# Performance work log

Hardware: AMD Instinct MI355X
Metric: run time of the kernel (lower is better)

## Reference

```python
import jax, jax.numpy as jnp
import numpy as np

D_MODEL = 1024
N_EXPERTS = 8
TOP_K = 2
B, S = 2, 2048


def setup_inputs() -> dict:
    key = jax.random.key(0)
    ks = jax.random.split(key, 12)
    d, e, h = D_MODEL, N_EXPERTS, 4 * D_MODEL
    sd = 1.0 / np.sqrt(d)
    sh = 1.0 / np.sqrt(h)
    return {
        "x": jax.random.normal(ks[0], (B, S, d), dtype=jnp.float32),
        "noise": jax.random.uniform(ks[1], (B, S, e), dtype=jnp.float32),
        # router linear [d, E]
        "Wr": jax.random.uniform(ks[2], (d, e), minval=-sd, maxval=sd),
        "br": jax.random.uniform(ks[3], (e,), minval=-sd, maxval=sd),
        # noise linear [d, E]
        "Wn": jax.random.uniform(ks[4], (d, e), minval=-sd, maxval=sd),
        "bn": jax.random.uniform(ks[5], (e,), minval=-sd, maxval=sd),
        # stacked expert FFN weights
        "W1": jax.random.uniform(ks[6], (e, d, h), minval=-sd, maxval=sd),
        "b1": jax.random.uniform(ks[7], (e, h), minval=-sd, maxval=sd),
        "W2": jax.random.uniform(ks[8], (e, h, d), minval=-sh, maxval=sh),
        "b2": jax.random.uniform(ks[9], (e, d), minval=-sh, maxval=sh),
    }


def _moe_forward(x, noise, Wr, br, Wn, bn, W1, b1, W2, b2):
    e = Wr.shape[-1]
    # noisy top-k router
    logits = x @ Wr + br + jax.nn.softplus(x @ Wn + bn) * noise  # [B,S,E]
    top_v, top_i = jax.lax.top_k(logits, TOP_K)                  # [B,S,K]
    # softmax over sparse top-k (non-topk entries are -inf -> weight 0)
    gates_k = jax.nn.softmax(top_v, axis=-1)                     # [B,S,K]
    gating = jnp.sum(jax.nn.one_hot(top_i, e, dtype=x.dtype) * gates_k[..., None], axis=-2)  # [B,S,E]
    # experts (dropout in eval mode = identity). Non-selected experts have
    # gate 0, so the dense weighted sum equals the masked gather/scatter.
    hdn = jax.nn.relu(jnp.einsum('bsd,edh->bseh', x, W1) + b1)   # [B,S,E,4d]
    y = jnp.einsum('bseh,ehd->bsed', hdn, W2) + b2               # [B,S,E,d]
    return jnp.einsum('bse,bsed->bsd', gating, y)


def reference(x, noise, Wr, br, Wn, bn, W1, b1, W2, b2):
    return _moe_forward(x, noise, Wr, br, Wn, bn, W1, b1, W2, b2)
```

## Files before the change

kernel.cpp:

```cpp
#include <hip/hip_runtime.h>
#include <hip/hip_bf16.h>
#include <cstdint>
#include <cstddef>

#define D_MODEL 1024
#define N_EXP   8
#define HID     4096
#define T_TOK   4096
#define NPAIR   (T_TOK * 2)
#define WSLOTS  72

#define WS_COUNTS   0
#define WS_CURSOR   32
#define WS_OFFSETS  64
#define WS_TOKE     128
#define WS_TOKG     32896
#define WS_LTOK     65664
#define WS_LGATE    98432
#define WS_XB       131328
#define WS_WB       (WS_XB + 8388608)
#define WS_H        (WS_WB + 67108864)

typedef __attribute__((ext_vector_type(8))) short bf16x8;
typedef __attribute__((ext_vector_type(4))) float f32x4;
typedef __attribute__((ext_vector_type(8))) unsigned short u16x8;
typedef unsigned short u16;

__device__ __forceinline__ u16 f2bf(float f) {
    unsigned u = __float_as_uint(f);
    u += 0x7FFFu + ((u >> 16) & 1u);
    return (u16)(u >> 16);
}

__device__ __forceinline__ void glds16(const void* g, void* l) {
    __builtin_amdgcn_global_load_lds(
        (const __attribute__((address_space(1))) void*)g,
        (__attribute__((address_space(3))) void*)l, 16, 0, 0);
}

__device__ __forceinline__ void chunk_map(int c, int& row, int& kc) {
    const int line = c >> 3, c8 = c & 7, u = c8 ^ (line & 7);
    row = line * 2 + (u >> 2);
    kc  = (u & 3) * 8;
}

__device__ __forceinline__ bool work_map(const int* counts, int w,
                                         int& e, int& m_t) {
    int tot = 0; e = -1; m_t = 0;
    #pragma unroll
    for (int i = 0; i < N_EXP; ++i) {
        const int tl = (counts[i] + 127) >> 7;
        if (e < 0 && w < tot + tl) { e = i; m_t = w - tot; }
        tot += tl;
    }
    return e >= 0;
}

__global__ __launch_bounds__(256) void k_router(
    const float* __restrict__ x, const float* __restrict__ noise,
    const float* __restrict__ Wr, const float* __restrict__ br,
    const float* __restrict__ Wn, const float* __restrict__ bn,
    int* __restrict__ counts, int* __restrict__ tok_e, float* __restrict__ tok_g,
    u16* __restrict__ xb)
{
    const int t   = blockIdx.x;
    const int tid = threadIdx.x;
    const int e   = tid & 7;
    const int g   = tid >> 3;
    const float* xr = x + (size_t)t * D_MODEL;

    {
        const float4 v4 = *(const float4*)(xr + tid * 4);
        ushort4 o;
        o.x = f2bf(v4.x); o.y = f2bf(v4.y); o.z = f2bf(v4.z); o.w = f2bf(v4.w);
        *(ushort4*)(xb + (size_t)t * D_MODEL + tid * 4) = o;
    }

    float ar = 0.f, an = 0.f;
    const int ibase = g * 32;
    #pragma unroll 8
    for (int j = 0; j < 32; ++j) {
        const int i = ibase + j;
        const float xv = xr[i];
        ar = fmaf(xv, Wr[i * 8 + e], ar);
        an = fmaf(xv, Wn[i * 8 + e], an);
    }

    __shared__ float sR[256], sN[256];
    sR[tid] = ar; sN[tid] = an;
    __syncthreads();
    for (int off = 128; off >= 8; off >>= 1) {
        if (tid < off) { sR[tid] += sR[tid + off]; sN[tid] += sN[tid + off]; }
        __syncthreads();
    }

    __shared__ float lg[8];
    if (tid < 8) {
        const float z  = sN[tid] + bn[tid];
        const float sp = fmaxf(z, 0.f) + log1pf(expf(-fabsf(z)));
        lg[tid] = sR[tid] + br[tid] + sp * noise[t * 8 + tid];
    }
    __syncthreads();

    if (tid == 0) {
        float v0 = -INFINITY, v1 = -INFINITY;
        int   i0 = 0,         i1 = 0;
        #pragma unroll
        for (int ee = 0; ee < 8; ++ee) {
            const float v = lg[ee];
            if (v > v0)      { v1 = v0; i1 = i0; v0 = v; i0 = ee; }
            else if (v > v1) { v1 = v;  i1 = ee; }
        }
        const float ew  = expf(v1 - v0);
        const float inv = 1.f / (1.f + ew);
        tok_e[t * 2 + 0] = i0;
        tok_e[t * 2 + 1] = i1;
        tok_g[t * 2 + 0] = inv;
        tok_g[t * 2 + 1] = ew * inv;
        atomicAdd(&counts[i0], 1);
        atomicAdd(&counts[i1], 1);
    }
}

__global__ void k_prefix(const int* __restrict__ counts, int* __restrict__ offsets)
{
    if (threadIdx.x == 0 && blockIdx.x == 0) {
        int acc = 0;
        #pragma unroll
        for (int e = 0; e < N_EXP; ++e) { offsets[e] = acc; acc += counts[e]; }
    }
}

__global__ __launch_bounds__(256) void k_scatter(
    const int* __restrict__ tok_e, const float* __restrict__ tok_g,
    const int* __restrict__ offsets, int* __restrict__ cursor,
    int* __restrict__ list_tok, float* __restrict__ list_gate)
{
    const int gid = blockIdx.x * 256 + threadIdx.x;
    if (gid >= NPAIR) return;
    const int e = tok_e[gid];
    const int p = atomicAdd(&cursor[e], 1);
    const int slot = offsets[e] + p;
    list_tok[slot]  = gid >> 1;
    list_gate[slot] = tok_g[gid];
}

__global__ __launch_bounds__(256) void k_cvtT(
    const float* __restrict__ in, u16* __restrict__ outp, int R, int C)
{
    const size_t esz = (size_t)R * C;
    const float* ine = in + (size_t)blockIdx.z * esz;
    u16* oute = outp + (size_t)blockIdx.z * esz;
    const int c0 = blockIdx.x * 32, r0 = blockIdx.y * 64;

    __shared__ u16 s[64 * 33];
    const int tid = threadIdx.x;
    const int lr = tid >> 3, lc = (tid & 7) * 4;
    #pragma unroll
    for (int p = 0; p < 2; ++p) {
        const int row = lr + p * 32;
        const float4 v = *(const float4*)(ine + (size_t)(r0 + row) * C + c0 + lc);
        s[row * 33 + lc + 0] = f2bf(v.x);
        s[row * 33 + lc + 1] = f2bf(v.y);
        s[row * 33 + lc + 2] = f2bf(v.z);
        s[row * 33 + lc + 3] = f2bf(v.w);
    }
    __syncthreads();
    const int oc = tid >> 3, rr = (tid & 7) * 8;
    u16x8 o;
    #pragma unroll
    for (int i = 0; i < 8; ++i) o[i] = s[(rr + i) * 33 + oc];
    *(u16x8*)(oute + (size_t)(c0 + oc) * R + r0 + rr) = o;
}

__global__ __launch_bounds__(256, 4) void k_ffn1(
    const u16* __restrict__ xb,
    const u16* __restrict__ W1t,
    const float* __restrict__ b1,
    const int* __restrict__ counts, const int* __restrict__ offsets,
    const int* __restrict__ list_tok,
    u16* __restrict__ H)
{
    const int bid = blockIdx.x;
    const int n_t = (bid & 7) | (((bid >> 3) & 3) << 3);
    const int wsl = bid >> 5;

    int e, m_t;
    if (!work_map(counts, wsl, e, m_t)) return;
    const int cnt  = counts[e];
    const int base = offsets[e];
    const int m0   = m_t * 128;
    const int n0   = n_t * 128;
    const u16* __restrict__ Be = W1t + (size_t)e * (HID * D_MODEL);

    __shared__ __align__(16) u16 SA[2 * 4096];
    __shared__ __align__(16) u16 SB[2 * 4096];
    __shared__ int stok[128];

    const int tid = threadIdx.x;
    if (tid < 128) stok[tid] = list_tok[base + min(m0 + tid, cnt - 1)];
    __syncthreads();

    int ar0, ak0, ar1, ak1;
    chunk_map(tid, ar0, ak0);
    chunk_map(tid + 256, ar1, ak1);
    const u16* Asrc0 = xb + (size_t)stok[ar0] * D_MODEL + ak0;
    const u16* Asrc1 = xb + (size_t)stok[ar1] * D_MODEL + ak1;
    const u16* Bsrc0 = Be + (size_t)(n0 + ar0) * D_MODEL + ak0;
    const u16* Bsrc1 = Be + (size_t)(n0 + ar1) * D_MODEL + ak1;

    const int lane = tid & 63, lr = lane & 15, hk = lane >> 4;
    const int w = tid >> 6, wm = w >> 1, wn = w & 1;
    const int colb  = ((((lr & 1) << 2) + hk) ^ (lr >> 1)) << 4;
    const int baseA = ((wm * 32 + (lr >> 1)) << 7) + colb;
    const int baseB = ((wn * 32 + (lr >> 1)) << 7) + colb;

    float bias[4];
    #pragma unroll
    for (int j = 0; j < 4; ++j) bias[j] = b1[(size_t)e * HID + n0 + wn * 64 + j * 16 + lr];

    f32x4 acc[4][4] = {};

    auto STAGE = [&](int s, int t) {
        const int kt = t * 32;
        char* Ab = (char*)SA + s * 8192;
        char* Bb = (char*)SB + s * 8192;
        glds16(Asrc0 + kt, Ab + tid * 16);
        glds16(Asrc1 + kt, Ab + (tid + 256) * 16);
        glds16(Bsrc0 + kt, Bb + tid * 16);
        glds16(Bsrc1 + kt, Bb + (tid + 256) * 16);
    };
    auto COMPUTE = [&](int s) {
        const char* Ab = (const char*)SA + s * 8192;
        const char* Bb = (const char*)SB + s * 8192;
        bf16x8 a[4], b[4];
        #pragma unroll
        for (int i = 0; i < 4; ++i) a[i] = *(const bf16x8*)(Ab + baseA + i * 1024);
        #pragma unroll
        for (int j = 0; j < 4; ++j) b[j] = *(const bf16x8*)(Bb + baseB + j * 1024);
        #pragma unroll
        for (int i = 0; i < 4; ++i)
            #pragma unroll
            for (int j = 0; j < 4; ++j)
                acc[i][j] = __builtin_amdgcn_mfma_f32_16x16x32_bf16(a[i], b[j], acc[i][j], 0, 0, 0);
    };

    const int NT = D_MODEL / 32;
    STAGE(0, 0);
    STAGE(1, 1);
    for (int t = 0; t < NT; ++t) {
        if (t < NT - 1) { asm volatile("s_waitcnt vmcnt(4)" ::: "memory"); }
        else            { asm volatile("s_waitcnt vmcnt(0)" ::: "memory"); }
        __builtin_amdgcn_s_barrier();
        __builtin_amdgcn_sched_barrier(0);
        COMPUTE(t & 1);
        __builtin_amdgcn_sched_barrier(0);
        __builtin_amdgcn_s_barrier();
        if (t + 2 < NT) STAGE(t & 1, t + 2);
    }

    #pragma unroll
    for (int i = 0; i < 4; ++i) {
        #pragma unroll
        for (int g = 0; g < 4; ++g) {
            const int m = m0 + wm * 64 + i * 16 + hk * 4 + g;
            if (m < cnt) {
                u16* dst = H + (size_t)(base + m) * HID + n0 + wn * 64 + lr;
                #pragma unroll
                for (int j = 0; j < 4; ++j)
                    dst[j * 16] = f2bf(fmaxf(acc[i][j][g] + bias[j], 0.f));
            }
        }
    }
}

__global__ __launch_bounds__(256, 4) void k_ffn2(
    const u16* __restrict__ Hb,
    const u16* __restrict__ W2t,
    const float* __restrict__ b2,
    const int* __restrict__ counts, const int* __restrict__ offsets,
    const int* __restrict__ list_tok, const float* __restrict__ list_gate,
    float* __restrict__ out)
{
    const int bid = blockIdx.x;
    const int n_t = bid & 7;
    const int wsl = bid >> 3;

    int e, m_t;
    if (!work_map(counts, wsl, e, m_t)) return;
    const int cnt  = counts[e];
    const int base = offsets[e];
    const int m0   = m_t * 128;
    const int n0   = n_t * 128;
    const u16* __restrict__ Be = W2t + (size_t)e * (D_MODEL * HID);

    __shared__ __align__(16) u16 SA[2 * 4096];
    __shared__ __align__(16) u16 SB[2 * 4096];
    __shared__ int   s_tok[128];
    __shared__ float s_gate[128];

    const int tid = threadIdx.x;
    if (tid < 128) {
        const int sl = base + min(m0 + tid, cnt - 1);
        s_tok[tid]  = list_tok[sl];
        s_gate[tid] = list_gate[sl];
    }
    __syncthreads();

    int ar0, ak0, ar1, ak1;
    chunk_map(tid, ar0, ak0);
    chunk_map(tid + 256, ar1, ak1);
    const u16* Asrc0 = Hb + (size_t)(base + min(m0 + ar0, cnt - 1)) * HID + ak0;
    const u16* Asrc1 = Hb + (size_t)(base + min(m0 + ar1, cnt - 1)) * HID + ak1;
    const u16* Bsrc0 = Be + (size_t)(n0 + ar0) * HID + ak0;
    const u16* Bsrc1 = Be + (size_t)(n0 + ar1) * HID + ak1;

    const int lane = tid & 63, lr = lane & 15, hk = lane >> 4;
    const int w = tid >> 6, wm = w >> 1, wn = w & 1;
    const int colb  = ((((lr & 1) << 2) + hk) ^ (lr >> 1)) << 4;
    const int baseA = ((wm * 32 + (lr >> 1)) << 7) + colb;
    const int baseB = ((wn * 32 + (lr >> 1)) << 7) + colb;

    float bias[4];
    #pragma unroll
    for (int j = 0; j < 4; ++j) bias[j] = b2[(size_t)e * D_MODEL + n0 + wn * 64 + j * 16 + lr];

    f32x4 acc[4][4] = {};

    auto STAGE = [&](int s, int t) {
        const int kt = t * 32;
        char* Ab = (char*)SA + s * 8192;
        char* Bb = (char*)SB + s * 8192;
        glds16(Asrc0 + kt, Ab + tid * 16);
        glds16(Asrc1 + kt, Ab + (tid + 256) * 16);
        glds16(Bsrc0 + kt, Bb + tid * 16);
        glds16(Bsrc1 + kt, Bb + (tid + 256) * 16);
    };
    auto COMPUTE = [&](int s) {
        const char* Ab = (const char*)SA + s * 8192;
        const char* Bb = (const char*)SB + s * 8192;
        bf16x8 a[4], b[4];
        #pragma unroll
        for (int i = 0; i < 4; ++i) a[i] = *(const bf16x8*)(Ab + baseA + i * 1024);
        #pragma unroll
        for (int j = 0; j < 4; ++j) b[j] = *(const bf16x8*)(Bb + baseB + j * 1024);
        #pragma unroll
        for (int i = 0; i < 4; ++i)
            #pragma unroll
            for (int j = 0; j < 4; ++j)
                acc[i][j] = __builtin_amdgcn_mfma_f32_16x16x32_bf16(a[i], b[j], acc[i][j], 0, 0, 0);
    };

    const int NT = HID / 32;
    STAGE(0, 0);
    STAGE(1, 1);
    for (int t = 0; t < NT; ++t) {
        if (t < NT - 1) { asm volatile("s_waitcnt vmcnt(4)" ::: "memory"); }
        else            { asm volatile("s_waitcnt vmcnt(0)" ::: "memory"); }
        __builtin_amdgcn_s_barrier();
        __builtin_amdgcn_sched_barrier(0);
        COMPUTE(t & 1);
        __builtin_amdgcn_sched_barrier(0);
        __builtin_amdgcn_s_barrier();
        if (t + 2 < NT) STAGE(t & 1, t + 2);
    }

    #pragma unroll
    for (int i = 0; i < 4; ++i) {
        #pragma unroll
        for (int g = 0; g < 4; ++g) {
            const int m = m0 + wm * 64 + i * 16 + hk * 4 + g;
            if (m < cnt) {
                const int   mm = m - m0;
                const int   tk = s_tok[mm];
                const float gt = s_gate[mm];
                float* dst = out + (size_t)tk * D_MODEL + n0 + wn * 64 + lr;
                #pragma unroll
                for (int j = 0; j < 4; ++j)
                    unsafeAtomicAdd(dst + j * 16, gt * (acc[i][j][g] + bias[j]));
            }
        }
    }
}

extern "C" void kernel_launch(void* const* d_in, const int* in_sizes, int n_in,
                              void* d_out, int out_size, void* d_ws, size_t ws_size,
                              hipStream_t stream)
{
    const float* x     = (const float*)d_in[0];
    const float* noise = (const float*)d_in[1];
    const float* Wr    = (const float*)d_in[2];
    const float* br    = (const float*)d_in[3];
    const float* Wn    = (const float*)d_in[4];
    const float* bn    = (const float*)d_in[5];
    const float* W1    = (const float*)d_in[6];
    const float* b1    = (const float*)d_in[7];
    const float* W2    = (const float*)d_in[8];
    const float* b2    = (const float*)d_in[9];
    float* out = (float*)d_out;

    char* ws = (char*)d_ws;
    int*   counts    = (int*)(ws + WS_COUNTS);
    int*   cursor    = (int*)(ws + WS_CURSOR);
    int*   offsets   = (int*)(ws + WS_OFFSETS);
    int*   tok_e     = (int*)(ws + WS_TOKE);
    float* tok_g     = (float*)(ws + WS_TOKG);
    int*   list_tok  = (int*)(ws + WS_LTOK);
    float* list_gate = (float*)(ws + WS_LGATE);
    u16*   xb        = (u16*)(ws + WS_XB);
    u16*   Wb        = (u16*)(ws + WS_WB);
    u16*   Hb        = (u16*)(ws + WS_H);

    hipMemsetAsync(ws, 0, 128, stream);
    hipMemsetAsync(d_out, 0, (size_t)out_size * sizeof(float), stream);

    k_cvtT<<<dim3(HID / 32, D_MODEL / 64, N_EXP), 256, 0, stream>>>(W1, Wb, D_MODEL, HID);
    k_router<<<T_TOK, 256, 0, stream>>>(x, noise, Wr, br, Wn, bn, counts, tok_e, tok_g, xb);
    k_prefix<<<1, 64, 0, stream>>>(counts, offsets);
    k_scatter<<<NPAIR / 256, 256, 0, stream>>>(tok_e, tok_g, offsets, cursor,
                                               list_tok, list_gate);

    k_ffn1<<<32 * WSLOTS, 256, 0, stream>>>(xb, Wb, b1, counts, offsets,
                                            list_tok, Hb);

    k_cvtT<<<dim3(D_MODEL / 32, HID / 64, N_EXP), 256, 0, stream>>>(W2, Wb, HID, D_MODEL);
    k_ffn2<<<8 * WSLOTS, 256, 0, stream>>>(Hb, Wb, b2, counts, offsets,
                                           list_tok, list_gate, out);
}
```

Before: 453.9 us.

## Enlarge FFN1 M-tile to 256 with 512 threads; deepen FFN2 K-step to 64

FFN1 now gives each block 256 token rows with 8 waves sharing one 128-column weight tile, so each W1 tile loaded into LDS is reused across twice as many tokens. FFN2 stages 64-wide K slices with a new XOR swizzle and makes two MFMA sub-steps per barrier, halving the number of barrier and wait rounds. The cost is more LDS per block, lower occupancy (launch bounds drop to 2 blocks per CU), and more padded rows wasted per expert when counts are not multiples of 256.

```diff
diff --git a/kernel.cpp b/kernel.cpp
--- a/kernel.cpp
+++ b/kernel.cpp
@@ -9,6 +9,7 @@
 #define T_TOK   4096
 #define NPAIR   (T_TOK * 2)
 #define WSLOTS  72
+#define WSL256  40
 
 #define WS_COUNTS   0
 #define WS_CURSOR   32
@@ -44,12 +45,24 @@
     kc  = (u & 3) * 8;
 }
 
+
 __device__ __forceinline__ bool work_map(const int* counts, int w,
                                          int& e, int& m_t) {
     int tot = 0; e = -1; m_t = 0;
     #pragma unroll
     for (int i = 0; i < N_EXP; ++i) {
         const int tl = (counts[i] + 127) >> 7;
+        if (e < 0 && w < tot + tl) { e = i; m_t = w - tot; }
+        tot += tl;
+    }
+    return e >= 0;
+}
+__device__ __forceinline__ bool work_map256(const int* counts, int w,
+                                            int& e, int& m_t) {
+    int tot = 0; e = -1; m_t = 0;
+    #pragma unroll
+    for (int i = 0; i < N_EXP; ++i) {
+        const int tl = (counts[i] + 255) >> 8;
         if (e < 0 && w < tot + tl) { e = i; m_t = w - tot; }
         tot += tl;
     }
@@ -173,7 +186,7 @@
     *(u16x8*)(oute + (size_t)(c0 + oc) * R + r0 + rr) = o;
 }
 
-__global__ __launch_bounds__(256, 4) void k_ffn1(
+__global__ __launch_bounds__(512, 2) void k_ffn1(
     const u16* __restrict__ xb,
     const u16* __restrict__ W1t,
     const float* __restrict__ b1,
@@ -186,28 +199,27 @@
     const int wsl = bid >> 5;
 
     int e, m_t;
-    if (!work_map(counts, wsl, e, m_t)) return;
+    if (!work_map256(counts, wsl, e, m_t)) return;
     const int cnt  = counts[e];
     const int base = offsets[e];
-    const int m0   = m_t * 128;
+    const int m0   = m_t * 256;
     const int n0   = n_t * 128;
     const u16* __restrict__ Be = W1t + (size_t)e * (HID * D_MODEL);
 
-    __shared__ __align__(16) u16 SA[2 * 4096];
+    __shared__ __align__(16) u16 SA[2 * 8192];
     __shared__ __align__(16) u16 SB[2 * 4096];
-    __shared__ int stok[128];
+    __shared__ int stok[256];
 
     const int tid = threadIdx.x;
-    if (tid < 128) stok[tid] = list_tok[base + min(m0 + tid, cnt - 1)];
+    if (tid < 256) stok[tid] = list_tok[base + min(m0 + tid, cnt - 1)];
     __syncthreads();
 
     int ar0, ak0, ar1, ak1;
     chunk_map(tid, ar0, ak0);
-    chunk_map(tid + 256, ar1, ak1);
+    chunk_map(tid + 512, ar1, ak1);
     const u16* Asrc0 = xb + (size_t)stok[ar0] * D_MODEL + ak0;
     const u16* Asrc1 = xb + (size_t)stok[ar1] * D_MODEL + ak1;
-    const u16* Bsrc0 = Be + (size_t)(n0 + ar0) * D_MODEL + ak0;
-    const u16* Bsrc1 = Be + (size_t)(n0 + ar1) * D_MODEL + ak1;
+    const u16* Bsrc  = Be + (size_t)(n0 + ar0) * D_MODEL + ak0;
 
     const int lane = tid & 63, lr = lane & 15, hk = lane >> 4;
     const int w = tid >> 6, wm = w >> 1, wn = w & 1;
@@ -223,16 +235,15 @@
 
     auto STAGE = [&](int s, int t) {
         const int kt = t * 32;
-        char* Ab = (char*)SA + s * 8192;
-        char* Bb = (char*)SB + s * 8192;
+        char* Ab = (char*)(SA + s * 8192);
+        char* Bb = (char*)(SB + s * 4096);
         glds16(Asrc0 + kt, Ab + tid * 16);
-        glds16(Asrc1 + kt, Ab + (tid + 256) * 16);
-        glds16(Bsrc0 + kt, Bb + tid * 16);
-        glds16(Bsrc1 + kt, Bb + (tid + 256) * 16);
+        glds16(Asrc1 + kt, Ab + (tid + 512) * 16);
+        glds16(Bsrc  + kt, Bb + tid * 16);
     };
     auto COMPUTE = [&](int s) {
-        const char* Ab = (const char*)SA + s * 8192;
-        const char* Bb = (const char*)SB + s * 8192;
+        const char* Ab = (const char*)(SA + s * 8192);
+        const char* Bb = (const char*)(SB + s * 4096);
         bf16x8 a[4], b[4];
         #pragma unroll
         for (int i = 0; i < 4; ++i) a[i] = *(const bf16x8*)(Ab + baseA + i * 1024);
@@ -249,7 +260,7 @@
     STAGE(0, 0);
     STAGE(1, 1);
     for (int t = 0; t < NT; ++t) {
-        if (t < NT - 1) { asm volatile("s_waitcnt vmcnt(4)" ::: "memory"); }
+        if (t < NT - 1) { asm volatile("s_waitcnt vmcnt(3)" ::: "memory"); }
         else            { asm volatile("s_waitcnt vmcnt(0)" ::: "memory"); }
         __builtin_amdgcn_s_barrier();
         __builtin_amdgcn_sched_barrier(0);
@@ -274,7 +285,7 @@
     }
 }
 
-__global__ __launch_bounds__(256, 4) void k_ffn2(
+__global__ __launch_bounds__(256, 2) void k_ffn2(
     const u16* __restrict__ Hb,
     const u16* __restrict__ W2t,
     const float* __restrict__ b2,
@@ -294,8 +305,8 @@
     const int n0   = n_t * 128;
     const u16* __restrict__ Be = W2t + (size_t)e * (D_MODEL * HID);
 
-    __shared__ __align__(16) u16 SA[2 * 4096];
-    __shared__ __align__(16) u16 SB[2 * 4096];
+    __shared__ __align__(16) u16 SA[2 * 8192];
+    __shared__ __align__(16) u16 SB[2 * 8192];
     __shared__ int   s_tok[128];
     __shared__ float s_gate[128];
 
@@ -307,19 +318,21 @@
     }
     __syncthreads();
 
-    int ar0, ak0, ar1, ak1;
-    chunk_map(tid, ar0, ak0);
-    chunk_map(tid + 256, ar1, ak1);
-    const u16* Asrc0 = Hb + (size_t)(base + min(m0 + ar0, cnt - 1)) * HID + ak0;
-    const u16* Asrc1 = Hb + (size_t)(base + min(m0 + ar1, cnt - 1)) * HID + ak1;
-    const u16* Bsrc0 = Be + (size_t)(n0 + ar0) * HID + ak0;
-    const u16* Bsrc1 = Be + (size_t)(n0 + ar1) * HID + ak1;
+    const u16* Asrc[4];
+    const u16* Bsrc[4];
+    #pragma unroll
+    for (int g = 0; g < 4; ++g) {
+        const int s = g * 256 + tid;
+        const int r = s >> 3;
+        const int u = (s & 7) ^ (r & 7);
+        Asrc[g] = Hb + (size_t)(base + min(m0 + r, cnt - 1)) * HID + u * 8;
+        Bsrc[g] = Be + (size_t)(n0 + r) * HID + u * 8;
+    }
 
     const int lane = tid & 63, lr = lane & 15, hk = lane >> 4;
     const int w = tid >> 6, wm = w >> 1, wn = w & 1;
-    const int colb  = ((((lr & 1) << 2) + hk) ^ (lr >> 1)) << 4;
-    const int baseA = ((wm * 32 + (lr >> 1)) << 7) + colb;
-    const int baseB = ((wn * 32 + (lr >> 1)) << 7) + colb;
+    const int baseA = (wm * 64 + lr) * 128 + ((hk ^ (lr & 7)) << 4);
+    const int baseB = (wn * 64 + lr) * 128 + ((hk ^ (lr & 7)) << 4);
 
     float bias[4];
     #pragma unroll
@@ -328,34 +341,38 @@
     f32x4 acc[4][4] = {};
 
     auto STAGE = [&](int s, int t) {
-        const int kt = t * 32;
-        char* Ab = (char*)SA + s * 8192;
-        char* Bb = (char*)SB + s * 8192;
-        glds16(Asrc0 + kt, Ab + tid * 16);
-        glds16(Asrc1 + kt, Ab + (tid + 256) * 16);
-        glds16(Bsrc0 + kt, Bb + tid * 16);
-        glds16(Bsrc1 + kt, Bb + (tid + 256) * 16);
+        const int kt = t * 64;
+        char* Ab = (char*)(SA + s * 8192);
+        char* Bb = (char*)(SB + s * 8192);
+        #pragma unroll
+        for (int g = 0; g < 4; ++g) glds16(Asrc[g] + kt, Ab + (g * 256 + tid) * 16);
+        #pragma unroll
+        for (int g = 0; g < 4; ++g) glds16(Bsrc[g] + kt, Bb + (g * 256 + tid) * 16);
     };
     auto COMPUTE = [&](int s) {
-        const char* Ab = (const char*)SA + s * 8192;
-        const char* Bb = (const char*)SB + s * 8192;
-        bf16x8 a[4], b[4];
-        #pragma unroll
-        for (int i = 0; i < 4; ++i) a[i] = *(const bf16x8*)(Ab + baseA + i * 1024);
-        #pragma unroll
-        for (int j = 0; j < 4; ++j) b[j] = *(const bf16x8*)(Bb + baseB + j * 1024);
-        #pragma unroll
-        for (int i = 0; i < 4; ++i)
+        const char* Ab = (const char*)(SA + s * 8192);
+        const char* Bb = (const char*)(SB + s * 8192);
+        #pragma unroll
+        for (int ks = 0; ks < 2; ++ks) {
+            const int kx = ks * 64;
+            bf16x8 a[4], b[4];
             #pragma unroll
-            for (int j = 0; j < 4; ++j)
-                acc[i][j] = __builtin_amdgcn_mfma_f32_16x16x32_bf16(a[i], b[j], acc[i][j], 0, 0, 0);
+            for (int i = 0; i < 4; ++i) a[i] = *(const bf16x8*)(Ab + ((baseA + i * 2048) ^ kx));
+            #pragma unroll
+            for (int j = 0; j < 4; ++j) b[j] = *(const bf16x8*)(Bb + ((baseB + j * 2048) ^ kx));
+            #pragma unroll
+            for (int i = 0; i < 4; ++i)
+                #pragma unroll
+                for (int j = 0; j < 4; ++j)
+                    acc[i][j] = __builtin_amdgcn_mfma_f32_16x16x32_bf16(a[i], b[j], acc[i][j], 0, 0, 0);
+        }
     };
 
-    const int NT = HID / 32;
+    const int NT = HID / 64;
     STAGE(0, 0);
     STAGE(1, 1);
     for (int t = 0; t < NT; ++t) {
-        if (t < NT - 1) { asm volatile("s_waitcnt vmcnt(4)" ::: "memory"); }
+        if (t < NT - 1) { asm volatile("s_waitcnt vmcnt(8)" ::: "memory"); }
         else            { asm volatile("s_waitcnt vmcnt(0)" ::: "memory"); }
         __builtin_amdgcn_s_barrier();
         __builtin_amdgcn_sched_barrier(0);
@@ -420,7 +437,7 @@
     k_scatter<<<NPAIR / 256, 256, 0, stream>>>(tok_e, tok_g, offsets, cursor,
                                                list_tok, list_gate);
 
-    k_ffn1<<<32 * WSLOTS, 256, 0, stream>>>(xb, Wb, b1, counts, offsets,
+    k_ffn1<<<32 * WSL256, 512, 0, stream>>>(xb, Wb, b1, counts, offsets,
                                             list_tok, Hb);
 
     k_cvtT<<<dim3(D_MODEL / 32, HID / 64, N_EXP), 256, 0, stream>>>(W2, Wb, HID, D_MODEL);
```

Result: slower. 502.8 us (+10.8%).

## Fuse fp32 weight conversion into expert GEMM B-tile loads

Applied to the files above, without the earlier changes.

Removes the two separate transpose-and-convert kernels that wrote bf16 copies of W1 and W2 to workspace. The FFN GEMMs now read fp32 weights directly through registers, pack them to bf16 with v_cvt_pk_bf16_f32 and write a padded LDS tile, pipelined one stage ahead. This avoids a full extra read and write pass over both weight tensors per call. In exchange, the GEMMs read weights at twice the byte width, every M-tile block repeats the conversion, and register and LDS pressure rise.

```diff
diff --git a/kernel.cpp b/kernel.cpp
--- a/kernel.cpp
+++ b/kernel.cpp
@@ -18,12 +18,10 @@
 #define WS_LTOK     65664
 #define WS_LGATE    98432
 #define WS_XB       131328
-#define WS_WB       (WS_XB + 8388608)
-#define WS_H        (WS_WB + 67108864)
+#define WS_H        (WS_XB + 8388608)
 
 typedef __attribute__((ext_vector_type(8))) short bf16x8;
 typedef __attribute__((ext_vector_type(4))) float f32x4;
-typedef __attribute__((ext_vector_type(8))) unsigned short u16x8;
 typedef unsigned short u16;
 
 __device__ __forceinline__ u16 f2bf(float f) {
@@ -145,37 +143,10 @@
     list_gate[slot] = tok_g[gid];
 }
 
-__global__ __launch_bounds__(256) void k_cvtT(
-    const float* __restrict__ in, u16* __restrict__ outp, int R, int C)
-{
-    const size_t esz = (size_t)R * C;
-    const float* ine = in + (size_t)blockIdx.z * esz;
-    u16* oute = outp + (size_t)blockIdx.z * esz;
-    const int c0 = blockIdx.x * 32, r0 = blockIdx.y * 64;
-
-    __shared__ u16 s[64 * 33];
-    const int tid = threadIdx.x;
-    const int lr = tid >> 3, lc = (tid & 7) * 4;
-    #pragma unroll
-    for (int p = 0; p < 2; ++p) {
-        const int row = lr + p * 32;
-        const float4 v = *(const float4*)(ine + (size_t)(r0 + row) * C + c0 + lc);
-        s[row * 33 + lc + 0] = f2bf(v.x);
-        s[row * 33 + lc + 1] = f2bf(v.y);
-        s[row * 33 + lc + 2] = f2bf(v.z);
-        s[row * 33 + lc + 3] = f2bf(v.w);
-    }
-    __syncthreads();
-    const int oc = tid >> 3, rr = (tid & 7) * 8;
-    u16x8 o;
-    #pragma unroll
-    for (int i = 0; i < 8; ++i) o[i] = s[(rr + i) * 33 + oc];
-    *(u16x8*)(oute + (size_t)(c0 + oc) * R + r0 + rr) = o;
-}
 
 __global__ __launch_bounds__(256, 4) void k_ffn1(
     const u16* __restrict__ xb,
-    const u16* __restrict__ W1t,
+    const float* __restrict__ W1,
     const float* __restrict__ b1,
     const int* __restrict__ counts, const int* __restrict__ offsets,
     const int* __restrict__ list_tok,
@@ -191,10 +162,10 @@
     const int base = offsets[e];
     const int m0   = m_t * 128;
     const int n0   = n_t * 128;
-    const u16* __restrict__ Be = W1t + (size_t)e * (HID * D_MODEL);
+    const float* __restrict__ Bw = W1 + (size_t)e * (D_MODEL * HID);
 
     __shared__ __align__(16) u16 SA[2 * 4096];
-    __shared__ __align__(16) u16 SB[2 * 4096];
+    __shared__ __align__(16) u16 SBl[2 * 5120];
     __shared__ int stok[128];
 
     const int tid = threadIdx.x;
@@ -206,38 +177,61 @@
     chunk_map(tid + 256, ar1, ak1);
     const u16* Asrc0 = xb + (size_t)stok[ar0] * D_MODEL + ak0;
     const u16* Asrc1 = xb + (size_t)stok[ar1] * D_MODEL + ak1;
-    const u16* Bsrc0 = Be + (size_t)(n0 + ar0) * D_MODEL + ak0;
-    const u16* Bsrc1 = Be + (size_t)(n0 + ar1) * D_MODEL + ak1;
+
+    const int kq = tid & 7;
+    const int nq = tid >> 3;
+    const float* Bbase = Bw + (size_t)(4 * kq) * HID + n0 + nq * 4;
 
     const int lane = tid & 63, lr = lane & 15, hk = lane >> 4;
     const int w = tid >> 6, wm = w >> 1, wn = w & 1;
     const int colb  = ((((lr & 1) << 2) + hk) ^ (lr >> 1)) << 4;
     const int baseA = ((wm * 32 + (lr >> 1)) << 7) + colb;
-    const int baseB = ((wn * 32 + (lr >> 1)) << 7) + colb;
+    const int baseBr = hk * 16;
 
     float bias[4];
     #pragma unroll
     for (int j = 0; j < 4; ++j) bias[j] = b1[(size_t)e * HID + n0 + wn * 64 + j * 16 + lr];
 
     f32x4 acc[4][4] = {};
-
-    auto STAGE = [&](int s, int t) {
+    float4 bv0, bv1, bv2, bv3;
+
+    auto ISSUE_B = [&](int t) {
+        const float* p = Bbase + (size_t)(t * 32) * HID;
+        bv0 = *(const float4*)(p);
+        bv1 = *(const float4*)(p + HID);
+        bv2 = *(const float4*)(p + 2 * HID);
+        bv3 = *(const float4*)(p + 3 * HID);
+    };
+    auto ISSUE_A = [&](int s, int t) {
         const int kt = t * 32;
         char* Ab = (char*)SA + s * 8192;
-        char* Bb = (char*)SB + s * 8192;
         glds16(Asrc0 + kt, Ab + tid * 16);
         glds16(Asrc1 + kt, Ab + (tid + 256) * 16);
-        glds16(Bsrc0 + kt, Bb + tid * 16);
-        glds16(Bsrc1 + kt, Bb + (tid + 256) * 16);
+    };
+    auto WRITE_B = [&](int s) {
+        char* Bb = (char*)SBl + s * 10240;
+        const float* f0 = (const float*)&bv0;
+        const float* f1 = (const float*)&bv1;
+        const float* f2 = (const float*)&bv2;
+        const float* f3 = (const float*)&bv3;
+        #pragma unroll
+        for (int c = 0; c < 4; ++c) {
+            unsigned p0, p1;
+            asm("v_cvt_pk_bf16_f32 %0, %1, %2" : "=v"(p0) : "v"(f0[c]), "v"(f1[c]));
+            asm("v_cvt_pk_bf16_f32 %0, %1, %2" : "=v"(p1) : "v"(f2[c]), "v"(f3[c]));
+            uint2 w2; w2.x = p0; w2.y = p1;
+            *(uint2*)(Bb + (4 * nq + c) * 80 + kq * 8) = w2;
+        }
     };
     auto COMPUTE = [&](int s) {
         const char* Ab = (const char*)SA + s * 8192;
-        const char* Bb = (const char*)SB + s * 8192;
+        const char* Bb = (const char*)SBl + s * 10240;
         bf16x8 a[4], b[4];
         #pragma unroll
         for (int i = 0; i < 4; ++i) a[i] = *(const bf16x8*)(Ab + baseA + i * 1024);
         #pragma unroll
-        for (int j = 0; j < 4; ++j) b[j] = *(const bf16x8*)(Bb + baseB + j * 1024);
+        for (int j = 0; j < 4; ++j)
+            b[j] = *(const bf16x8*)(Bb + (wn * 64 + j * 16 + lr) * 80 + baseBr);
         #pragma unroll
         for (int i = 0; i < 4; ++i)
             #pragma unroll
@@ -246,17 +240,36 @@
     };
 
     const int NT = D_MODEL / 32;
-    STAGE(0, 0);
-    STAGE(1, 1);
+    __builtin_amdgcn_sched_barrier(0);
+    ISSUE_B(0);
+    __builtin_amdgcn_sched_barrier(0);
+    ISSUE_A(0, 0);
+    __builtin_amdgcn_sched_barrier(0);
+    asm volatile("s_waitcnt vmcnt(2)" ::: "memory");
+    WRITE_B(0);
+    __builtin_amdgcn_sched_barrier(0);
+    ISSUE_B(1);
+    __builtin_amdgcn_sched_barrier(0);
+    ISSUE_A(1, 1);
+    __builtin_amdgcn_sched_barrier(0);
+
     for (int t = 0; t < NT; ++t) {
-        if (t < NT - 1) { asm volatile("s_waitcnt vmcnt(4)" ::: "memory"); }
-        else            { asm volatile("s_waitcnt vmcnt(0)" ::: "memory"); }
+        if (t < NT - 1) { asm volatile("s_waitcnt vmcnt(2) lgkmcnt(0)" ::: "memory"); }
+        else            { asm volatile("s_waitcnt vmcnt(0) lgkmcnt(0)" ::: "memory"); }
         __builtin_amdgcn_s_barrier();
         __builtin_amdgcn_sched_barrier(0);
+        if (t + 1 < NT) WRITE_B((t + 1) & 1);
+        __builtin_amdgcn_sched_barrier(0);
         COMPUTE(t & 1);
         __builtin_amdgcn_sched_barrier(0);
         __builtin_amdgcn_s_barrier();
-        if (t + 2 < NT) STAGE(t & 1, t + 2);
+        if (t + 2 < NT) {
+            __builtin_amdgcn_sched_barrier(0);
+            ISSUE_B(t + 2);
+            __builtin_amdgcn_sched_barrier(0);
+            ISSUE_A(t & 1, t + 2);
+            __builtin_amdgcn_sched_barrier(0);
+        }
     }
 
     #pragma unroll
@@ -276,7 +289,7 @@
 
 __global__ __launch_bounds__(256, 4) void k_ffn2(
     const u16* __restrict__ Hb,
-    const u16* __restrict__ W2t,
+    const float* __restrict__ W2,
     const float* __restrict__ b2,
     const int* __restrict__ counts, const int* __restrict__ offsets,
     const int* __restrict__ list_tok, const float* __restrict__ list_gate,
@@ -292,10 +305,10 @@
     const int base = offsets[e];
     const int m0   = m_t * 128;
     const int n0   = n_t * 128;
-    const u16* __restrict__ Be = W2t + (size_t)e * (D_MODEL * HID);
+    const float* __restrict__ Bw = W2 + (size_t)e * (HID * D_MODEL);
 
     __shared__ __align__(16) u16 SA[2 * 4096];
-    __shared__ __align__(16) u16 SB[2 * 4096];
+    __shared__ __align__(16) u16 SBl[2 * 5120];
     __shared__ int   s_tok[128];
     __shared__ float s_gate[128];
 
@@ -312,38 +325,61 @@
     chunk_map(tid + 256, ar1, ak1);
     const u16* Asrc0 = Hb + (size_t)(base + min(m0 + ar0, cnt - 1)) * HID + ak0;
     const u16* Asrc1 = Hb + (size_t)(base + min(m0 + ar1, cnt - 1)) * HID + ak1;
-    const u16* Bsrc0 = Be + (size_t)(n0 + ar0) * HID + ak0;
-    const u16* Bsrc1 = Be + (size_t)(n0 + ar1) * HID + ak1;
+
+    const int kq = tid & 7;
+    const int nq = tid >> 3;
+    const float* Bbase = Bw + (size_t)(4 * kq) * D_MODEL + n0 + nq * 4;
 
     const int lane = tid & 63, lr = lane & 15, hk = lane >> 4;
     const int w = tid >> 6, wm = w >> 1, wn = w & 1;
     const int colb  = ((((lr & 1) << 2) + hk) ^ (lr >> 1)) << 4;
     const int baseA = ((wm * 32 + (lr >> 1)) << 7) + colb;
-    const int baseB = ((wn * 32 + (lr >> 1)) << 7) + colb;
+    const int baseBr = hk * 16;
 
     float bias[4];
     #pragma unroll
     for (int j = 0; j < 4; ++j) bias[j] = b2[(size_t)e * D_MODEL + n0 + wn * 64 + j * 16 + lr];
 
     f32x4 acc[4][4] = {};
-
-    auto STAGE = [&](int s, int t) {
+    float4 bv0, bv1, bv2, bv3;
+
+    auto ISSUE_B = [&](int t) {
+        const float* p = Bbase + (size_t)(t * 32) * D_MODEL;
+        bv0 = *(const float4*)(p);
+        bv1 = *(const float4*)(p + D_MODEL);
+        bv2 = *(const float4*)(p + 2 * D_MODEL);
+        bv3 = *(const float4*)(p + 3 * D_MODEL);
+    };
+    auto ISSUE_A = [&](int s, int t) {
         const int kt = t * 32;
         char* Ab = (char*)SA + s * 8192;
-        char* Bb = (char*)SB + s * 8192;
         glds16(Asrc0 + kt, Ab + tid * 16);
         glds16(Asrc1 + kt, Ab + (tid + 256) * 16);
-        glds16(Bsrc0 + kt, Bb + tid * 16);
-        glds16(Bsrc1 + kt, Bb + (tid + 256) * 16);
+    };
+    auto WRITE_B = [&](int s) {
+        char* Bb = (char*)SBl + s * 10240;
+        const float* f0 = (const float*)&bv0;
+        const float* f1 = (const float*)&bv1;
+        const float* f2 = (const float*)&bv2;
+        const float* f3 = (const float*)&bv3;
+        #pragma unroll
+        for (int c = 0; c < 4; ++c) {
+            unsigned p0, p1;
+            asm("v_cvt_pk_bf16_f32 %0, %1, %2" : "=v"(p0) : "v"(f0[c]), "v"(f1[c]));
+            asm("v_cvt_pk_bf16_f32 %0, %1, %2" : "=v"(p1) : "v"(f2[c]), "v"(f3[c]));
+            uint2 w2; w2.x = p0; w2.y = p1;
+            *(uint2*)(Bb + (4 * nq + c) * 80 + kq * 8) = w2;
+        }
     };
     auto COMPUTE = [&](int s) {
         const char* Ab = (const char*)SA + s * 8192;
-        const char* Bb = (const char*)SB + s * 8192;
+        const char* Bb = (const char*)SBl + s * 10240;
         bf16x8 a[4], b[4];
         #pragma unroll
         for (int i = 0; i < 4; ++i) a[i] = *(const bf16x8*)(Ab + baseA + i * 1024);
         #pragma unroll
-        for (int j = 0; j < 4; ++j) b[j] = *(const bf16x8*)(Bb + baseB + j * 1024);
+        for (int j = 0; j < 4; ++j)
+            b[j] = *(const bf16x8*)(Bb + (wn * 64 + j * 16 + lr) * 80 + baseBr);
         #pragma unroll
         for (int i = 0; i < 4; ++i)
             #pragma unroll
@@ -352,17 +388,36 @@
     };
 
     const int NT = HID / 32;
-    STAGE(0, 0);
-    STAGE(1, 1);
+    __builtin_amdgcn_sched_barrier(0);
+    ISSUE_B(0);
+    __builtin_amdgcn_sched_barrier(0);
+    ISSUE_A(0, 0);
+    __builtin_amdgcn_sched_barrier(0);
+    asm volatile("s_waitcnt vmcnt(2)" ::: "memory");
+    WRITE_B(0);
+    __builtin_amdgcn_sched_barrier(0);
+    ISSUE_B(1);
+    __builtin_amdgcn_sched_barrier(0);
+    ISSUE_A(1, 1);
+    __builtin_amdgcn_sched_barrier(0);
+
     for (int t = 0; t < NT; ++t) {
-        if (t < NT - 1) { asm volatile("s_waitcnt vmcnt(4)" ::: "memory"); }
-        else            { asm volatile("s_waitcnt vmcnt(0)" ::: "memory"); }
+        if (t < NT - 1) { asm volatile("s_waitcnt vmcnt(2) lgkmcnt(0)" ::: "memory"); }
+        else            { asm volatile("s_waitcnt vmcnt(0) lgkmcnt(0)" ::: "memory"); }
         __builtin_amdgcn_s_barrier();
         __builtin_amdgcn_sched_barrier(0);
+        if (t + 1 < NT) WRITE_B((t + 1) & 1);
+        __builtin_amdgcn_sched_barrier(0);
         COMPUTE(t & 1);
         __builtin_amdgcn_sched_barrier(0);
         __builtin_amdgcn_s_barrier();
-        if (t + 2 < NT) STAGE(t & 1, t + 2);
+        if (t + 2 < NT) {
+            __builtin_amdgcn_sched_barrier(0);
+            ISSUE_B(t + 2);
+            __builtin_amdgcn_sched_barrier(0);
+            ISSUE_A(t & 1, t + 2);
+            __builtin_amdgcn_sched_barrier(0);
+        }
     }
 
     #pragma unroll
@@ -408,22 +463,19 @@
     int*   list_tok  = (int*)(ws + WS_LTOK);
     float* list_gate = (float*)(ws + WS_LGATE);
     u16*   xb        = (u16*)(ws + WS_XB);
-    u16*   Wb        = (u16*)(ws + WS_WB);
     u16*   Hb        = (u16*)(ws + WS_H);
 
     hipMemsetAsync(ws, 0, 128, stream);
     hipMemsetAsync(d_out, 0, (size_t)out_size * sizeof(float), stream);
 
-    k_cvtT<<<dim3(HID / 32, D_MODEL / 64, N_EXP), 256, 0, stream>>>(W1, Wb, D_MODEL, HID);
-    k_router<<<T_TOK, 256, 0, stream>>>(x, noise, Wr, br, Wn, bn, counts, tok_e, tok_g, xb);
+    k_router<<<T_TOK, 256, 0, stream>>>(x, noise, Wr, br, Wn, bn,
+                                        counts, tok_e, tok_g, xb);
     k_prefix<<<1, 64, 0, stream>>>(counts, offsets);
     k_scatter<<<NPAIR / 256, 256, 0, stream>>>(tok_e, tok_g, offsets, cursor,
                                                list_tok, list_gate);
 
-    k_ffn1<<<32 * WSLOTS, 256, 0, stream>>>(xb, Wb, b1, counts, offsets,
+    k_ffn1<<<32 * WSLOTS, 256, 0, stream>>>(xb, W1, b1, counts, offsets,
                                             list_tok, Hb);
-
-    k_cvtT<<<dim3(D_MODEL / 32, HID / 64, N_EXP), 256, 0, stream>>>(W2, Wb, HID, D_MODEL);
-    k_ffn2<<<8 * WSLOTS, 256, 0, stream>>>(Hb, Wb, b2, counts, offsets,
+    k_ffn2<<<8 * WSLOTS, 256, 0, stream>>>(Hb, W2, b2, counts, offsets,
                                            list_tok, list_gate, out);
 }
```

Result: slower. 588.5 us (+29.7%).
